# Performance work log

Measured on AMD Instinct MI355X. Metric: run time of the kernel, lower is better.

Reference implementation:

```python
import jax, jax.numpy as jnp
import numpy as np

C_IN = 1024
C_INTER = 512  # in_channels // 2, canonical NONLocalBlock default
N_CLASSES = 13


def setup_inputs() -> dict:
    key = jax.random.key(0)
    ks = jax.random.split(key, 11)
    B, T, H, W = 16, 8, 14, 14
    s = 0.02
    return {
        "x": jax.random.normal(ks[0], (B, C_IN, T, H, W), dtype=jnp.float32),
        # 1x1x1 conv projections stored as [out, in] matrices + biases
        "g_w": jax.random.normal(ks[1], (C_INTER, C_IN), dtype=jnp.float32) * s,
        "g_b": jnp.zeros((C_INTER,), dtype=jnp.float32),
        "theta_w": jax.random.normal(ks[2], (C_INTER, C_IN), dtype=jnp.float32) * s,
        "theta_b": jnp.zeros((C_INTER,), dtype=jnp.float32),
        "phi_w": jax.random.normal(ks[3], (C_INTER, C_IN), dtype=jnp.float32) * s,
        "phi_b": jnp.zeros((C_INTER,), dtype=jnp.float32),
        "w_w": jax.random.normal(ks[4], (C_IN, C_INTER), dtype=jnp.float32) * s,
        "w_b": jnp.zeros((C_IN,), dtype=jnp.float32),
        "fc_w": jax.random.normal(ks[5], (N_CLASSES, C_IN), dtype=jnp.float32) * s,
        "fc_b": jnp.zeros((N_CLASSES,), dtype=jnp.float32),
    }


def reference(x, g_w, g_b, theta_w, theta_b, phi_w, phi_b, w_w, w_b, fc_w, fc_b):
    B, C, T, H, W = x.shape
    xf = x.reshape(B, C, -1)  # [B, C, N], N = T*H*W
    # 1x1x1 conv projections == channel matmuls
    g = jnp.einsum('oc,bcn->bno', g_w, xf) + g_b        # [B, N, 512]
    th = jnp.einsum('oc,bcn->bno', theta_w, xf) + theta_b  # [B, N, 512]
    ph = jnp.einsum('oc,bcn->bno', phi_w, xf) + phi_b      # [B, N, 512]
    # pairwise affinity (embedded Gaussian): [B, N, N]
    f = jnp.einsum('bnd,bmd->bnm', th, ph)
    attn = jax.nn.softmax(f, axis=-1)
    y = jnp.einsum('bnm,bmd->bnd', attn, g)             # [B, N, 512]
    wy = jnp.einsum('cd,bnd->bcn', w_w, y) + w_b[None, :, None]  # [B, C, N]
    z = wy.reshape(B, C, T, H, W) + x                    # residual
    pooled = z.mean(axis=(2, 3, 4))                      # adaptive avgpool (1,1,1)
    return pooled @ fc_w.T + fc_b                        # [B, 13]
```

## Files before the change

kernel.cpp:

```cpp
#include <hip/hip_runtime.h>
#include <hip/hip_bf16.h>


#define BATCH 16
#define CIN   1024
#define CINT  512
#define NSP   1568
#define NPAD  1664
#define NTIL  13
#define NCLS  13

using bf16 = __hip_bfloat16;
typedef __attribute__((ext_vector_type(8))) short short8;
typedef __attribute__((ext_vector_type(4))) float f32x4;

#define DEVI static __device__ __forceinline__

DEVI void gload16(const void* g, void* l) {
  __builtin_amdgcn_global_load_lds((const __attribute__((address_space(1))) void*)g,
                                   (__attribute__((address_space(3))) void*)l, 16, 0, 0);
}

DEVI float wave_sum(float v) {
#pragma unroll
  for (int m = 32; m; m >>= 1) v += __shfl_xor(v, m);
  return v;
}

DEVI short f2bf(float f) {
  union { __hip_bfloat16 h; short s; } u;
  u.h = __float2bfloat16(f);
  return u.s;
}
DEVI float bf2f(short s) {
  union { float f; unsigned u; } x;
  x.u = ((unsigned)(unsigned short)s) << 16;
  return x.f;
}

__global__ __launch_bounds__(256) void k_transpose(const float* __restrict__ x,
                                                   bf16* __restrict__ xt,
                                                   float* __restrict__ xbar) {
  __shared__ float t[128 * 37];
  const int b = blockIdx.z;
  const int n0 = blockIdx.x * 32;
  const int c0 = blockIdx.y * 128;
  const int tid = threadIdx.x;
  const int lane = tid & 63;
  const float* xb = x + (size_t)b * CIN * NSP;
  const bool pad = (n0 >= NSP);
#pragma unroll
  for (int it = 0; it < 4; ++it) {
    const int slot = it * 256 + tid;
    const int cr = slot >> 3;
    const int q = slot & 7;
    float4 v = {0.f, 0.f, 0.f, 0.f};
    if (!pad) v = *(const float4*)(xb + (size_t)(c0 + cr) * NSP + n0 + q * 4);
    t[cr * 37 + q * 4 + 0] = v.x;
    t[cr * 37 + q * 4 + 1] = v.y;
    t[cr * 37 + q * 4 + 2] = v.z;
    t[cr * 37 + q * 4 + 3] = v.w;
    float s = v.x + v.y + v.z + v.w;
    s += __shfl_xor(s, 1);
    s += __shfl_xor(s, 2);
    s += __shfl_xor(s, 4);
    if ((lane & 7) == 0 && !pad)
      atomicAdd(&xbar[b * CIN + c0 + cr], s * (1.0f / NSP));
  }
  __syncthreads();
  bf16* xo = xt + (size_t)b * NPAD * CIN;
#pragma unroll
  for (int it = 0; it < 2; ++it) {
    const int slot = it * 256 + tid;
    const int n = slot >> 4;
    const int seg = slot & 15;
    short8 o;
#pragma unroll
    for (int k = 0; k < 8; ++k) o[k] = f2bf(t[(seg * 8 + k) * 37 + n]);
    *(short8*)(xo + (size_t)(n0 + n) * CIN + c0 + seg * 8) = o;
  }
}

__global__ void k_wconv(const float* __restrict__ thw, const float* __restrict__ phw,
                        bf16* __restrict__ wb) {
  const int i4 = (blockIdx.x * 256 + threadIdx.x) * 4;
  const float* s = (i4 < 512 * 1024) ? (thw + i4) : (phw + (i4 - 512 * 1024));
  const float4 v = *(const float4*)s;
  wb[i4 + 0] = __float2bfloat16(v.x);
  wb[i4 + 1] = __float2bfloat16(v.y);
  wb[i4 + 2] = __float2bfloat16(v.z);
  wb[i4 + 3] = __float2bfloat16(v.w);
}

template <int LDK>
DEVI void gemm128_bt(const bf16* Ag, const bf16* Bg, bf16* lds,
                     f32x4 acc[4][4]) {
  const int tid = threadIdx.x;
  const int lane = tid & 63;
  const int w = tid >> 6;
  const int wr = (w >> 1) * 64;
  const int wc = (w & 1) * 64;
  const int kc_src8 = ((lane & 3) ^ ((lane >> 3) & 3)) * 8;
  const int kc_rd8 = (((lane >> 4) ^ ((lane >> 1) & 3))) * 8;
  constexpr int NT = LDK / 32;

  auto STAGE = [&](int buf, int ks) {
    bf16* lA = lds + buf * 8192;
    bf16* lB = lA + 4096;
#pragma unroll
    for (int it = 0; it < 2; ++it) {
      const int ch = w * 64 + it * 256 + lane;
      const int row = ch >> 2;
      const int lbase = (w * 64 + it * 256) * 8;
      gload16(Ag + (size_t)row * LDK + ks * 32 + kc_src8, lA + lbase);
      gload16(Bg + (size_t)row * LDK + ks * 32 + kc_src8, lB + lbase);
    }
  };
  auto COMPUTE = [&](int buf) {
    const bf16* lA = lds + buf * 8192;
    const bf16* lB = lA + 4096;
    short8 af[4], bfr[4];
#pragma unroll
    for (int i = 0; i < 4; ++i)
      af[i] = *(const short8*)(lA + (wr + i * 16 + (lane & 15)) * 32 + kc_rd8);
#pragma unroll
    for (int i = 0; i < 4; ++i)
      bfr[i] = *(const short8*)(lB + (wc + i * 16 + (lane & 15)) * 32 + kc_rd8);
#pragma unroll
    for (int m = 0; m < 4; ++m)
#pragma unroll
      for (int n = 0; n < 4; ++n)
        acc[m][n] = __builtin_amdgcn_mfma_f32_16x16x32_bf16(af[m], bfr[n], acc[m][n], 0, 0, 0);
  };

  STAGE(0, 0);
  __syncthreads();
  int ks = 0;
#pragma unroll 1
  while (ks < NT - 2) {
    STAGE(1, ks + 1);
    COMPUTE(0);
    __syncthreads();
    STAGE(0, ks + 2);
    COMPUTE(1);
    __syncthreads();
    ks += 2;
  }
  STAGE(1, NT - 1);
  COMPUTE(0);
  __syncthreads();
  COMPUTE(1);
}

__global__ __launch_bounds__(256) void k_proj(const bf16* __restrict__ xt,
                                              const bf16* __restrict__ wb,
                                              const float* __restrict__ thb,
                                              const float* __restrict__ phb,
                                              bf16* __restrict__ th,
                                              bf16* __restrict__ ph) {
  __shared__ bf16 smem[16384];
  const int id = blockIdx.x;
  const int rcls = id & 7;
  const int q = id >> 3;
  const int bm = (q >> 3) * 8 + rcls;
  const int bo = q & 7;

  f32x4 acc[4][4];
  const f32x4 z = {0.f, 0.f, 0.f, 0.f};
#pragma unroll
  for (int m = 0; m < 4; ++m)
#pragma unroll
    for (int n = 0; n < 4; ++n) acc[m][n] = z;

  gemm128_bt<CIN>(xt + (size_t)bm * 128 * CIN, wb + (size_t)bo * 128 * CIN,
                  smem, acc);

  const int tid = threadIdx.x;
  const int lane = tid & 63;
  const int w = tid >> 6;
  const int wr = (w >> 1) * 64;
  const int wc = (w & 1) * 64;
  const float* bias = (bo < 4) ? thb : phb;
  bf16* outb = (bo < 4) ? th : ph;
  const int obase = (bo & 3) * 128;
  __syncthreads();
#pragma unroll
  for (int m = 0; m < 4; ++m)
#pragma unroll
    for (int n = 0; n < 4; ++n) {
      const int col = wc + n * 16 + (lane & 15);
      const float bv = bias[obase + col];
#pragma unroll
      for (int j = 0; j < 4; ++j) {
        const int row = wr + m * 16 + (lane >> 4) * 4 + j;
        smem[row * 128 + (col ^ ((row & 7) << 3))] =
            __float2bfloat16(acc[m][n][j] + bv);
      }
    }
  __syncthreads();
#pragma unroll
  for (int it = 0; it < 8; ++it) {
    const int slot = it * 256 + tid;
    const int r = slot >> 4;
    const int seg = slot & 15;
    const short8 v = *(const short8*)(smem + r * 128 + ((seg ^ (r & 7)) << 3));
    *(short8*)(outb + (size_t)(bm * 128 + r) * CINT + obase + seg * 8) = v;
  }
}

__global__ __launch_bounds__(256) void k_fgemm(const bf16* __restrict__ th,
                                               const bf16* __restrict__ ph,
                                               bf16* __restrict__ eb,
                                               float* __restrict__ psum) {
  __shared__ bf16 smem[16384];
  __shared__ float rsum2[2][128];
  const int id = blockIdx.x;
  const int rcls = id & 7;
  const int q = id >> 3;
  const int bloc = q / 169;
  const int t = q - bloc * 169;
  const int b = bloc * 8 + rcls;
  const int bm = t / 13;
  const int bn = t - bm * 13;

  f32x4 acc[4][4];
  const f32x4 z = {0.f, 0.f, 0.f, 0.f};
#pragma unroll
  for (int m = 0; m < 4; ++m)
#pragma unroll
    for (int n = 0; n < 4; ++n) acc[m][n] = z;

  gemm128_bt<CINT>(th + ((size_t)b * NPAD + bm * 128) * CINT,
                   ph + ((size_t)b * NPAD + bn * 128) * CINT,
                   smem, acc);

  const int tid = threadIdx.x;
  const int lane = tid & 63;
  const int w = tid >> 6;
  const int wr = (w >> 1) * 64;
  const int wc = (w & 1) * 64;
  bf16* ebb = eb + ((size_t)b * NPAD + bm * 128) * NPAD + bn * 128;
  __syncthreads();
#pragma unroll
  for (int m = 0; m < 4; ++m)
#pragma unroll
    for (int j = 0; j < 4; ++j) {
      const int row = wr + m * 16 + (lane >> 4) * 4 + j;
      float ps = 0.f;
#pragma unroll
      for (int n = 0; n < 4; ++n) {
        const int col = wc + n * 16 + (lane & 15);
        const float ev = __expf(acc[m][n][j]);
        smem[row * 128 + (col ^ ((row & 7) << 3))] = __float2bfloat16(ev);
        if (bn * 128 + col < NSP) ps += ev;
      }
      ps += __shfl_xor(ps, 1);
      ps += __shfl_xor(ps, 2);
      ps += __shfl_xor(ps, 4);
      ps += __shfl_xor(ps, 8);
      if ((lane & 15) == 0) rsum2[w & 1][row] = ps;
    }
  __syncthreads();
  if (tid < 128)
    psum[((size_t)b * NTIL + bn) * NPAD + bm * 128 + tid] =
        rsum2[0][tid] + rsum2[1][tid];
#pragma unroll
  for (int it = 0; it < 8; ++it) {
    const int slot = it * 256 + tid;
    const int r = slot >> 4;
    const int seg = slot & 15;
    const short8 v = *(const short8*)(smem + r * 128 + ((seg ^ (r & 7)) << 3));
    *(short8*)(ebb + (size_t)r * NPAD + seg * 8) = v;
  }
}

__global__ void k_recip(const float* __restrict__ psum, float* __restrict__ rinv) {
  const int id = blockIdx.x * 256 + threadIdx.x;
  const int b = id / NSP;
  const int n = id - b * NSP;
  float s = 0.f;
#pragma unroll
  for (int t = 0; t < NTIL; ++t) s += psum[((size_t)b * NTIL + t) * NPAD + n];
  rinv[id] = 1.0f / s;
}

__global__ void k_abar(const bf16* __restrict__ eb, const float* __restrict__ rinv,
                       float* __restrict__ abar) {
  const int b = blockIdx.y;
  const int n0 = blockIdx.x * 49;
  const int m0 = threadIdx.x * 8;
  if (m0 >= NSP) return;
  const bf16* fb = eb + (size_t)b * NPAD * NPAD;
  float a[8];
#pragma unroll
  for (int k = 0; k < 8; ++k) a[k] = 0.f;
#pragma unroll 1
  for (int n = n0; n < n0 + 49; ++n) {
    const float iS = rinv[b * NSP + n];
    const short8 v = *(const short8*)(fb + (size_t)n * NPAD + m0);
#pragma unroll
    for (int k = 0; k < 8; ++k) a[k] += bf2f(v[k]) * iS;
  }
#pragma unroll
  for (int k = 0; k < 8; ++k)
    atomicAdd(&abar[b * NSP + m0 + k], a[k] * (1.0f / NSP));
}

__global__ __launch_bounds__(128) void k_xg(const bf16* __restrict__ xt,
                                            const float* __restrict__ abar,
                                            float* __restrict__ xg) {
  const int b = blockIdx.y;
  const int n0 = blockIdx.x * 98;
  const int c0 = threadIdx.x * 8;
  const bf16* xb = xt + (size_t)b * NPAD * CIN;
  float a[8];
#pragma unroll
  for (int k = 0; k < 8; ++k) a[k] = 0.f;
#pragma unroll 1
  for (int n = n0; n < n0 + 98; ++n) {
    const float wgt = abar[b * NSP + n];
    const short8 v = *(const short8*)(xb + (size_t)n * CIN + c0);
#pragma unroll
    for (int k = 0; k < 8; ++k) a[k] += bf2f(v[k]) * wgt;
  }
#pragma unroll
  for (int k = 0; k < 8; ++k)
    atomicAdd(&xg[b * CIN + c0 + k], a[k]);
}

__global__ __launch_bounds__(64) void k_ybar(const float* __restrict__ gw,
                                             const float* __restrict__ gb,
                                             const float* __restrict__ xg,
                                             float* __restrict__ syb) {
  const int d = blockIdx.x;
  const int lane = threadIdx.x;
  const float4* wr = (const float4*)(gw + (size_t)d * CIN);
  float4 wv[4];
#pragma unroll
  for (int k = 0; k < 4; ++k) wv[k] = wr[k * 64 + lane];
  const float bv = gb[d];
#pragma unroll 1
  for (int b = 0; b < BATCH; ++b) {
    const float4* xr = (const float4*)(xg + (size_t)b * CIN);
    float s = 0.f;
#pragma unroll
    for (int k = 0; k < 4; ++k) {
      const float4 xv = xr[k * 64 + lane];
      s += wv[k].x * xv.x + wv[k].y * xv.y + wv[k].z * xv.z + wv[k].w * xv.w;
    }
    s = wave_sum(s);
    if (lane == 0) syb[b * CINT + d] = s + bv;
  }
}

__global__ __launch_bounds__(64) void k_spool(const float* __restrict__ ww,
                                              const float* __restrict__ wbias,
                                              const float* __restrict__ xbar,
                                              const float* __restrict__ syb,
                                              float* __restrict__ spool) {
  const int c = blockIdx.x;
  const int lane = threadIdx.x;
  const float4* wr = (const float4*)(ww + (size_t)c * CINT);
  float4 wv[2];
#pragma unroll
  for (int k = 0; k < 2; ++k) wv[k] = wr[k * 64 + lane];
  const float bv = wbias[c];
#pragma unroll 1
  for (int b = 0; b < BATCH; ++b) {
    const float4* yr = (const float4*)(syb + (size_t)b * CINT);
    float s = 0.f;
#pragma unroll
    for (int k = 0; k < 2; ++k) {
      const float4 yv = yr[k * 64 + lane];
      s += wv[k].x * yv.x + wv[k].y * yv.y + wv[k].z * yv.z + wv[k].w * yv.w;
    }
    s = wave_sum(s);
    if (lane == 0) spool[b * CIN + c] = s + bv + xbar[b * CIN + c];
  }
}

__global__ __launch_bounds__(64) void k_out(const float* __restrict__ spool,
                                            const float* __restrict__ fcw,
                                            const float* __restrict__ fcb,
                                            float* __restrict__ out) {
  const int b = blockIdx.x;
  const int lane = threadIdx.x;
  const float4* pr = (const float4*)(spool + (size_t)b * CIN);
  float4 pv[4];
#pragma unroll
  for (int k = 0; k < 4; ++k) pv[k] = pr[k * 64 + lane];
#pragma unroll 1
  for (int cls = 0; cls < NCLS; ++cls) {
    const float4* wr = (const float4*)(fcw + (size_t)cls * CIN);
    float s = 0.f;
#pragma unroll
    for (int k = 0; k < 4; ++k) {
      const float4 wv = wr[k * 64 + lane];
      s += wv.x * pv[k].x + wv.y * pv[k].y + wv.z * pv[k].z + wv.w * pv[k].w;
    }
    s = wave_sum(s);
    if (lane == 0) out[b * NCLS + cls] = s + fcb[cls];
  }
}

extern "C" void kernel_launch(void* const* d_in, const int* in_sizes, int n_in,
                              void* d_out, int out_size, void* d_ws, size_t ws_size,
                              hipStream_t stream) {
  const float* x    = (const float*)d_in[0];
  const float* g_w  = (const float*)d_in[1];
  const float* g_b  = (const float*)d_in[2];
  const float* th_w = (const float*)d_in[3];
  const float* th_b = (const float*)d_in[4];
  const float* ph_w = (const float*)d_in[5];
  const float* ph_b = (const float*)d_in[6];
  const float* w_w  = (const float*)d_in[7];
  const float* w_b  = (const float*)d_in[8];
  const float* fc_w = (const float*)d_in[9];
  const float* fc_b = (const float*)d_in[10];
  float* out = (float*)d_out;

  char* ws = (char*)d_ws;
  size_t off = 0;
  auto carve = [&](size_t bytes) {
    void* p = ws + off;
    off = (off + bytes + 255) & ~(size_t)255;
    return p;
  };
  bf16*  xt    = (bf16*)carve((size_t)BATCH * NPAD * CIN * 2);
  bf16*  wb    = (bf16*)carve((size_t)1024 * 1024 * 2);
  bf16*  th    = (bf16*)carve((size_t)BATCH * NPAD * CINT * 2);
  bf16*  ph    = (bf16*)carve((size_t)BATCH * NPAD * CINT * 2);
  bf16*  eb    = (bf16*)carve((size_t)BATCH * NPAD * NPAD * 2);
  float* psum  = (float*)carve((size_t)BATCH * NTIL * NPAD * 4);
  float* rinv  = (float*)carve((size_t)BATCH * NSP * 4);
  float* abar  = (float*)carve((size_t)BATCH * NSP * 4);
  float* xbar  = (float*)carve((size_t)BATCH * CIN * 4);
  float* xg    = (float*)carve((size_t)BATCH * CIN * 4);
  float* syb   = (float*)carve((size_t)BATCH * CINT * 4);
  float* spool = (float*)carve((size_t)BATCH * CIN * 4);
  (void)ws_size; (void)in_sizes; (void)n_in; (void)out_size;

  hipMemsetAsync(abar, 0, (size_t)BATCH * NSP * 4, stream);
  hipMemsetAsync(xbar, 0, (size_t)BATCH * CIN * 4, stream);
  hipMemsetAsync(xg,   0, (size_t)BATCH * CIN * 4, stream);

  k_transpose<<<dim3(52, 8, 16), 256, 0, stream>>>(x, xt, xbar);
  k_wconv<<<1024, 256, 0, stream>>>(th_w, ph_w, wb);
  k_proj<<<1664, 256, 0, stream>>>(xt, wb, th_b, ph_b, th, ph);
  k_fgemm<<<2704, 256, 0, stream>>>(th, ph, eb, psum);
  k_recip<<<98, 256, 0, stream>>>(psum, rinv);
  k_abar<<<dim3(32, 16), 256, 0, stream>>>(eb, rinv, abar);
  k_xg<<<dim3(16, 16), 128, 0, stream>>>(xt, abar, xg);
  k_ybar<<<512, 64, 0, stream>>>(g_w, g_b, xg, syb);
  k_spool<<<1024, 64, 0, stream>>>(w_w, w_b, xbar, syb, spool);
  k_out<<<16, 64, 0, stream>>>(spool, fc_w, fc_b, out);
}
```

Measured before the change: 297.1 us.

## Fold recip into abar, move xbar sum into xg, skip padded tile stores

Removes the separate k_recip launch: each k_abar block now computes the reciprocal softmax denominators for its 49 rows into shared memory. The xbar channel mean moves out of k_transpose, dropping its per-row atomics, and is accumulated alongside the weighted sum in k_xg, which already reads every xt row. k_proj and k_fgemm skip stores for padded rows and columns in the last tile, cutting global write traffic. The cost is a little redundant psum reading across abar blocks and an extra register accumulator in k_xg.

```diff
diff --git a/kernel.cpp b/kernel.cpp
--- a/kernel.cpp
+++ b/kernel.cpp
@@ -39,14 +39,12 @@
 }
 
 __global__ __launch_bounds__(256) void k_transpose(const float* __restrict__ x,
-                                                   bf16* __restrict__ xt,
-                                                   float* __restrict__ xbar) {
+                                                   bf16* __restrict__ xt) {
   __shared__ float t[128 * 37];
   const int b = blockIdx.z;
   const int n0 = blockIdx.x * 32;
   const int c0 = blockIdx.y * 128;
   const int tid = threadIdx.x;
-  const int lane = tid & 63;
   const float* xb = x + (size_t)b * CIN * NSP;
   const bool pad = (n0 >= NSP);
 #pragma unroll
@@ -60,12 +58,6 @@
     t[cr * 37 + q * 4 + 1] = v.y;
     t[cr * 37 + q * 4 + 2] = v.z;
     t[cr * 37 + q * 4 + 3] = v.w;
-    float s = v.x + v.y + v.z + v.w;
-    s += __shfl_xor(s, 1);
-    s += __shfl_xor(s, 2);
-    s += __shfl_xor(s, 4);
-    if ((lane & 7) == 0 && !pad)
-      atomicAdd(&xbar[b * CIN + c0 + cr], s * (1.0f / NSP));
   }
   __syncthreads();
   bf16* xo = xt + (size_t)b * NPAD * CIN;
@@ -183,6 +175,7 @@
   const float* bias = (bo < 4) ? thb : phb;
   bf16* outb = (bo < 4) ? th : ph;
   const int obase = (bo & 3) * 128;
+  const bool mtail = (bm % 13) == 12;
   __syncthreads();
 #pragma unroll
   for (int m = 0; m < 4; ++m)
@@ -203,6 +196,7 @@
     const int slot = it * 256 + tid;
     const int r = slot >> 4;
     const int seg = slot & 15;
+    if (mtail && r >= 32) continue;
     const short8 v = *(const short8*)(smem + r * 128 + ((seg ^ (r & 7)) << 3));
     *(short8*)(outb + (size_t)(bm * 128 + r) * CINT + obase + seg * 8) = v;
   }
@@ -261,7 +255,7 @@
       if ((lane & 15) == 0) rsum2[w & 1][row] = ps;
     }
   __syncthreads();
-  if (tid < 128)
+  if (tid < 128 && (bm != 12 || tid < 32))
     psum[((size_t)b * NTIL + bn) * NPAD + bm * 128 + tid] =
         rsum2[0][tid] + rsum2[1][tid];
 #pragma unroll
@@ -269,26 +263,28 @@
     const int slot = it * 256 + tid;
     const int r = slot >> 4;
     const int seg = slot & 15;
+    if (bm == 12 && r >= 32) continue;
+    if (bn == 12 && seg >= 4) continue;
     const short8 v = *(const short8*)(smem + r * 128 + ((seg ^ (r & 7)) << 3));
     *(short8*)(ebb + (size_t)r * NPAD + seg * 8) = v;
   }
 }
 
-__global__ void k_recip(const float* __restrict__ psum, float* __restrict__ rinv) {
-  const int id = blockIdx.x * 256 + threadIdx.x;
-  const int b = id / NSP;
-  const int n = id - b * NSP;
-  float s = 0.f;
-#pragma unroll
-  for (int t = 0; t < NTIL; ++t) s += psum[((size_t)b * NTIL + t) * NPAD + n];
-  rinv[id] = 1.0f / s;
-}
-
-__global__ void k_abar(const bf16* __restrict__ eb, const float* __restrict__ rinv,
+__global__ void k_abar(const bf16* __restrict__ eb, const float* __restrict__ psum,
                        float* __restrict__ abar) {
+  __shared__ float srinv[49];
   const int b = blockIdx.y;
   const int n0 = blockIdx.x * 49;
-  const int m0 = threadIdx.x * 8;
+  const int tid = threadIdx.x;
+  if (tid < 49) {
+    float s = 0.f;
+#pragma unroll
+    for (int t = 0; t < NTIL; ++t)
+      s += psum[((size_t)b * NTIL + t) * NPAD + n0 + tid];
+    srinv[tid] = 1.0f / s;
+  }
+  __syncthreads();
+  const int m0 = tid * 8;
   if (m0 >= NSP) return;
   const bf16* fb = eb + (size_t)b * NPAD * NPAD;
   float a[8];
@@ -296,7 +292,7 @@
   for (int k = 0; k < 8; ++k) a[k] = 0.f;
 #pragma unroll 1
   for (int n = n0; n < n0 + 49; ++n) {
-    const float iS = rinv[b * NSP + n];
+    const float iS = srinv[n - n0];
     const short8 v = *(const short8*)(fb + (size_t)n * NPAD + m0);
 #pragma unroll
     for (int k = 0; k < 8; ++k) a[k] += bf2f(v[k]) * iS;
@@ -308,24 +304,31 @@
 
 __global__ __launch_bounds__(128) void k_xg(const bf16* __restrict__ xt,
                                             const float* __restrict__ abar,
-                                            float* __restrict__ xg) {
+                                            float* __restrict__ xg,
+                                            float* __restrict__ xbar) {
   const int b = blockIdx.y;
   const int n0 = blockIdx.x * 98;
   const int c0 = threadIdx.x * 8;
   const bf16* xb = xt + (size_t)b * NPAD * CIN;
-  float a[8];
-#pragma unroll
-  for (int k = 0; k < 8; ++k) a[k] = 0.f;
+  float a[8], s[8];
+#pragma unroll
+  for (int k = 0; k < 8; ++k) { a[k] = 0.f; s[k] = 0.f; }
 #pragma unroll 1
   for (int n = n0; n < n0 + 98; ++n) {
     const float wgt = abar[b * NSP + n];
     const short8 v = *(const short8*)(xb + (size_t)n * CIN + c0);
 #pragma unroll
-    for (int k = 0; k < 8; ++k) a[k] += bf2f(v[k]) * wgt;
-  }
-#pragma unroll
-  for (int k = 0; k < 8; ++k)
+    for (int k = 0; k < 8; ++k) {
+      const float f = bf2f(v[k]);
+      a[k] += f * wgt;
+      s[k] += f;
+    }
+  }
+#pragma unroll
+  for (int k = 0; k < 8; ++k) {
     atomicAdd(&xg[b * CIN + c0 + k], a[k]);
+    atomicAdd(&xbar[b * CIN + c0 + k], s[k] * (1.0f / NSP));
+  }
 }
 
 __global__ __launch_bounds__(64) void k_ybar(const float* __restrict__ gw,
@@ -432,7 +435,6 @@
   bf16*  ph    = (bf16*)carve((size_t)BATCH * NPAD * CINT * 2);
   bf16*  eb    = (bf16*)carve((size_t)BATCH * NPAD * NPAD * 2);
   float* psum  = (float*)carve((size_t)BATCH * NTIL * NPAD * 4);
-  float* rinv  = (float*)carve((size_t)BATCH * NSP * 4);
   float* abar  = (float*)carve((size_t)BATCH * NSP * 4);
   float* xbar  = (float*)carve((size_t)BATCH * CIN * 4);
   float* xg    = (float*)carve((size_t)BATCH * CIN * 4);
@@ -444,13 +446,12 @@
   hipMemsetAsync(xbar, 0, (size_t)BATCH * CIN * 4, stream);
   hipMemsetAsync(xg,   0, (size_t)BATCH * CIN * 4, stream);
 
-  k_transpose<<<dim3(52, 8, 16), 256, 0, stream>>>(x, xt, xbar);
+  k_transpose<<<dim3(52, 8, 16), 256, 0, stream>>>(x, xt);
   k_wconv<<<1024, 256, 0, stream>>>(th_w, ph_w, wb);
   k_proj<<<1664, 256, 0, stream>>>(xt, wb, th_b, ph_b, th, ph);
   k_fgemm<<<2704, 256, 0, stream>>>(th, ph, eb, psum);
-  k_recip<<<98, 256, 0, stream>>>(psum, rinv);
-  k_abar<<<dim3(32, 16), 256, 0, stream>>>(eb, rinv, abar);
-  k_xg<<<dim3(16, 16), 128, 0, stream>>>(xt, abar, xg);
+  k_abar<<<dim3(32, 16), 256, 0, stream>>>(eb, psum, abar);
+  k_xg<<<dim3(16, 16), 128, 0, stream>>>(xt, abar, xg, xbar);
   k_ybar<<<512, 64, 0, stream>>>(g_w, g_b, xg, syb);
   k_spool<<<1024, 64, 0, stream>>>(w_w, w_b, xbar, syb, spool);
   k_out<<<16, 64, 0, stream>>>(spool, fc_w, fc_b, out);
```

Result: slower. 313.4 us (+5.5%).
